# Kernel tuning notes

Measured on AMD Instinct MI355X. Metric: run time of the kernel, lower is better.

The kernel has to match this reference:

```python
import jax, jax.numpy as jnp
import numpy as np

H, I, BS = 4096, 14336, 128   # hidden, intermediate, quant blocksize
B, S = 4, 2048                # batch, seq_len


def _dequant(w_int, s, blocksize):
    # w_int: [in, out] int8-valued weights; s: [in//blocksize, out] per-block scales.
    # Each contiguous block of `blocksize` input rows shares one scale.
    return w_int.astype(jnp.float32) * jnp.repeat(s, blocksize, axis=0)


def setup_inputs() -> dict:
    key = jax.random.key(0)
    k = jax.random.split(key, 7)
    x = jax.random.normal(k[0], (B, S, H), dtype=jnp.float32)
    w0 = jax.random.randint(k[1], (H, I), -127, 128, dtype=jnp.int32)  # gate proj (int8 values)
    w1 = jax.random.randint(k[2], (H, I), -127, 128, dtype=jnp.int32)  # up proj
    w2 = jax.random.randint(k[3], (I, H), -127, 128, dtype=jnp.int32)  # down proj
    # small positive per-block scales, typical magnitude for int8 weight quant
    s0 = jax.random.uniform(k[4], (H // BS, I), dtype=jnp.float32) * 0.02 + 1e-3
    s1 = jax.random.uniform(k[5], (H // BS, I), dtype=jnp.float32) * 0.02 + 1e-3
    s2 = jax.random.uniform(k[6], (I // BS, H), dtype=jnp.float32) * 0.02 + 1e-3
    return {"x": x, "w0": w0, "w1": w1, "w2": w2,
            "s0": s0, "s1": s1, "s2": s2, "blocksize": BS}


def reference(x, w0, w1, w2, s0, s1, s2, blocksize):
    # Fused w8a16 gated MLP: out = (silu(x @ W0) * (x @ W1)) @ W2
    W0 = _dequant(w0, s0, blocksize)  # [H, I]
    W1 = _dequant(w1, s1, blocksize)  # [H, I]
    W2 = _dequant(w2, s2, blocksize)  # [I, H]
    g = jnp.einsum('bsh,hi->bsi', x, W0)   # gate
    u = jnp.einsum('bsh,hi->bsi', x, W1)   # up
    h = jax.nn.silu(g) * u                 # [B, S, I]
    return jnp.einsum('bsi,ih->bsh', h, W2)  # same shape as x
```

## Files before the change

kernel.cpp:

```cpp
#include <hip/hip_runtime.h>
#include <cstdint>

#define H_DIM 4096
#define I_DIM 14336
#define M_TOT 8192
#define NI_DIM (2 * I_DIM)

typedef __bf16 bf16_t;
typedef bf16_t bf16x8_t __attribute__((ext_vector_type(8)));
typedef float f32x4_t __attribute__((ext_vector_type(4)));

#define AS1 __attribute__((address_space(1)))
#define AS3 __attribute__((address_space(3)))

static __device__ __forceinline__ unsigned short f2bf(float f) {
  union { float f; unsigned int u; } v; v.f = f;
  unsigned int r = ((v.u >> 16) & 1u) + 0x7FFFu;
  return (unsigned short)((v.u + r) >> 16);
}

static __device__ __forceinline__ void gl2lds16(const void* g, void* l) {
  __builtin_amdgcn_global_load_lds((AS1 void*)(void*)g, (AS3 void*)l, 16, 0, 0);
}

__global__ void k_cvt_x(const float* __restrict__ x,
                        unsigned short* __restrict__ xb, long n4) {
  long i = (long)blockIdx.x * blockDim.x + threadIdx.x;
  const long stride = (long)gridDim.x * blockDim.x;
  for (; i < n4; i += stride) {
    float4 v = ((const float4*)x)[i];
    ushort4 o;
    o.x = f2bf(v.x); o.y = f2bf(v.y); o.z = f2bf(v.z); o.w = f2bf(v.w);
    ((ushort4*)xb)[i] = o;
  }
}

__global__ void k_dequant_t(const int* __restrict__ w, const float* __restrict__ s,
                            unsigned short* __restrict__ wt, int K, int N,
                            int ioff) {
  __shared__ __align__(16) float tile[64 * 68];
  const int n0 = blockIdx.x * 64;
  const int k0 = blockIdx.y * 64;
  const int t = threadIdx.x;
  const int tx = t & 15;
  const int ty = t >> 4;
#pragma unroll
  for (int i = 0; i < 4; ++i) {
    const long gk = k0 + i * 16 + ty;
    const int4 wv = *(const int4*)(w + gk * N + (n0 + tx * 4));
    const float4 sv = *(const float4*)(s + (gk >> 7) * (long)N + (n0 + tx * 4));
    float4 o;
    o.x = (float)wv.x * sv.x;
    o.y = (float)wv.y * sv.y;
    o.z = (float)wv.z * sv.z;
    o.w = (float)wv.w * sv.w;
    *(float4*)(&tile[(i * 16 + ty) * 68 + tx * 4]) = o;
  }
  __syncthreads();
  const int nl = t >> 2;
  const int kc = (t & 3) << 4;
  unsigned int pk[8];
#pragma unroll
  for (int j = 0; j < 8; ++j) {
    unsigned int lo = f2bf(tile[(kc + 2 * j) * 68 + nl]);
    unsigned int hi = f2bf(tile[(kc + 2 * j + 1) * 68 + nl]);
    pk[j] = lo | (hi << 16);
  }
  const int n = n0 + nl;
  const long orow = (ioff < 0) ? (long)n
                               : (long)(((n >> 4) << 5) + (n & 15) + ioff);
  const long base = orow * K + (k0 + kc);
  uint4* dst = (uint4*)(wt + base);
  dst[0] = make_uint4(pk[0], pk[1], pk[2], pk[3]);
  dst[1] = make_uint4(pk[4], pk[5], pk[6], pk[7]);
}

template <int KDIM, int EPI>
__global__ __launch_bounds__(512, 2) void k_gemm8(
    const unsigned short* __restrict__ A,
    const unsigned short* __restrict__ B,
    void* __restrict__ Cout, int Ntiles) {
  __shared__ __align__(16) unsigned short lds[65536];
  constexpr int KT = KDIM / 64;

  const int nwg = 32 * Ntiles;
  int id = blockIdx.x;
  id = (id & 7) * (nwg >> 3) + (id >> 3);
  const int per = 16 * Ntiles;
  const int grp = id / per;
  const int wi = id - grp * per;
  const int mt = grp * 16 + (wi & 15);
  const int nt = wi >> 4;
  const long m0 = (long)mt * 256;
  const long n0 = (long)nt * 256;

  const int t = threadIdx.x;
  const int lane = t & 63;
  const int wave = t >> 6;
  const int wm = wave >> 2;
  const int wn = wave & 3;

  const int srow = lane >> 3;
  const int scol = ((lane & 7) ^ srow) << 3;
  const unsigned short* pA = A + (m0 + wave * 16 + srow) * (long)KDIM + scol;
  const unsigned short* pB = B + (n0 + wave * 16 + srow) * (long)KDIM + scol;
  const int ldst = wave * 1024;

  const int lr = lane & 15;
  const int pch = ((lane >> 4) ^ (lane & 7)) << 3;
  int aof[4], bof[4];
#pragma unroll
  for (int mi = 0; mi < 4; ++mi)
    aof[mi] = wm * 8192 + (mi * 16 + lr) * 64 + pch;
#pragma unroll
  for (int nj = 0; nj < 4; ++nj)
    bof[nj] = 16384 + (wn >> 1) * 8192 +
              ((wn & 1) * 64 + nj * 16 + lr) * 64 + pch;

  auto stgA = [&](int tile, int half, int buf) {
    const long go = (long)half * 128 * KDIM + (long)tile * 64;
    unsigned short* d = &lds[buf * 32768 + half * 8192 + ldst];
    gl2lds16(pA + go, d);
    gl2lds16(pA + go + 8 * (long)KDIM, d + 512);
  };
  auto stgB = [&](int tile, int half, int buf) {
    const long go = (long)half * 128 * KDIM + (long)tile * 64;
    unsigned short* d = &lds[buf * 32768 + 16384 + half * 8192 + ldst];
    gl2lds16(pB + go, d);
    gl2lds16(pB + go + 8 * (long)KDIM, d + 512);
  };

  f32x4_t acc[8][4];
  const f32x4_t fz = {0.f, 0.f, 0.f, 0.f};
#pragma unroll
  for (int mi = 0; mi < 8; ++mi)
#pragma unroll
    for (int nj = 0; nj < 4; ++nj) acc[mi][nj] = fz;

  stgB(0, 0, 0); stgB(0, 1, 0);
  stgA(0, 0, 0); stgA(0, 1, 0);
  stgB(1, 0, 1); stgB(1, 1, 1);
  asm volatile("s_waitcnt vmcnt(4)" ::: "memory");
  __builtin_amdgcn_s_barrier();

  bf16x8_t af[4][2], b0[2][2], b1[2][2];

  for (int kt = 0; kt < KT; ++kt) {
    const int cb = kt & 1;
    const unsigned short* lb = &lds[cb * 32768];
    const bool pa = (kt + 1 < KT);
    const bool pb = (kt + 2 < KT);

#pragma unroll
    for (int mi = 0; mi < 4; ++mi) {
      af[mi][0] = *(const bf16x8_t*)(lb + aof[mi]);
      af[mi][1] = *(const bf16x8_t*)(lb + (aof[mi] ^ 32));
    }
#pragma unroll
    for (int nj = 0; nj < 2; ++nj) {
      b0[nj][0] = *(const bf16x8_t*)(lb + bof[nj]);
      b0[nj][1] = *(const bf16x8_t*)(lb + (bof[nj] ^ 32));
    }
    if (pa) stgA(kt + 1, 0, cb ^ 1);
    __builtin_amdgcn_s_barrier();
    asm volatile("s_waitcnt lgkmcnt(0)" ::: "memory");
    __builtin_amdgcn_sched_barrier(0);
    __builtin_amdgcn_s_setprio(1);
#pragma unroll
    for (int mi = 0; mi < 4; ++mi)
#pragma unroll
      for (int nj = 0; nj < 2; ++nj)
#pragma unroll
        for (int ks = 0; ks < 2; ++ks)
          acc[mi][nj] = __builtin_amdgcn_mfma_f32_16x16x32_bf16(
              af[mi][ks], b0[nj][ks], acc[mi][nj], 0, 0, 0);
    __builtin_amdgcn_s_setprio(0);
    __builtin_amdgcn_s_barrier();

#pragma unroll
    for (int nj = 0; nj < 2; ++nj) {
      b1[nj][0] = *(const bf16x8_t*)(lb + bof[2 + nj]);
      b1[nj][1] = *(const bf16x8_t*)(lb + (bof[2 + nj] ^ 32));
    }
    if (pa) stgA(kt + 1, 1, cb ^ 1);
    __builtin_amdgcn_s_barrier();
    asm volatile("s_waitcnt lgkmcnt(0)" ::: "memory");
    __builtin_amdgcn_sched_barrier(0);
    __builtin_amdgcn_s_setprio(1);
#pragma unroll
    for (int mi = 0; mi < 4; ++mi)
#pragma unroll
      for (int nj = 0; nj < 2; ++nj)
#pragma unroll
        for (int ks = 0; ks < 2; ++ks)
          acc[mi][2 + nj] = __builtin_amdgcn_mfma_f32_16x16x32_bf16(
              af[mi][ks], b1[nj][ks], acc[mi][2 + nj], 0, 0, 0);
    __builtin_amdgcn_s_setprio(0);
    __builtin_amdgcn_s_barrier();

#pragma unroll
    for (int mi = 0; mi < 4; ++mi) {
      af[mi][0] = *(const bf16x8_t*)(lb + (aof[mi] + 4096));
      af[mi][1] = *(const bf16x8_t*)(lb + ((aof[mi] + 4096) ^ 32));
    }
    if (pb) stgB(kt + 2, 0, cb);
    __builtin_amdgcn_s_barrier();
    asm volatile("s_waitcnt lgkmcnt(0)" ::: "memory");
    __builtin_amdgcn_sched_barrier(0);
    __builtin_amdgcn_s_setprio(1);
#pragma unroll
    for (int mi = 0; mi < 4; ++mi)
#pragma unroll
      for (int nj = 0; nj < 2; ++nj)
#pragma unroll
        for (int ks = 0; ks < 2; ++ks)
          acc[4 + mi][2 + nj] = __builtin_amdgcn_mfma_f32_16x16x32_bf16(
              af[mi][ks], b1[nj][ks], acc[4 + mi][2 + nj], 0, 0, 0);
    __builtin_amdgcn_s_setprio(0);
    __builtin_amdgcn_s_barrier();

    if (pb) stgB(kt + 2, 1, cb);
    __builtin_amdgcn_s_barrier();
    __builtin_amdgcn_s_setprio(1);
#pragma unroll
    for (int mi = 0; mi < 4; ++mi)
#pragma unroll
      for (int nj = 0; nj < 2; ++nj)
#pragma unroll
        for (int ks = 0; ks < 2; ++ks)
          acc[4 + mi][nj] = __builtin_amdgcn_mfma_f32_16x16x32_bf16(
              af[mi][ks], b0[nj][ks], acc[4 + mi][nj], 0, 0, 0);
    __builtin_amdgcn_s_setprio(0);
    if (pb)
      asm volatile("s_waitcnt vmcnt(4)" ::: "memory");
    else if (pa)
      asm volatile("s_waitcnt vmcnt(0)" ::: "memory");
    __builtin_amdgcn_s_barrier();
  }

  const long mr0 = m0 + wm * 128 + ((lane >> 4) << 2);
  if constexpr (EPI == 1) {
    unsigned short* h = (unsigned short*)Cout;
    const long col0 = (n0 >> 1) + wn * 32 + (lane & 15);
#pragma unroll
    for (int mi = 0; mi < 8; ++mi) {
#pragma unroll
      for (int k = 0; k < 2; ++k) {
        const long c = col0 + k * 16;
#pragma unroll
        for (int r = 0; r < 4; ++r) {
          const float gg = acc[mi][2 * k][r];
          const float uu = acc[mi][2 * k + 1][r];
          const float sg = gg / (1.0f + __expf(-gg));
          h[(mr0 + mi * 16 + r) * (long)I_DIM + c] = f2bf(sg * uu);
        }
      }
    }
  } else {
    float* o = (float*)Cout;
    const long col0 = n0 + wn * 64 + (lane & 15);
#pragma unroll
    for (int mi = 0; mi < 8; ++mi)
#pragma unroll
      for (int nj = 0; nj < 4; ++nj)
#pragma unroll
        for (int r = 0; r < 4; ++r)
          o[(mr0 + mi * 16 + r) * (long)H_DIM + (col0 + nj * 16)] =
              acc[mi][nj][r];
  }
}

extern "C" void kernel_launch(void* const* d_in, const int* in_sizes, int n_in,
                              void* d_out, int out_size, void* d_ws, size_t ws_size,
                              hipStream_t stream) {
  const float* x  = (const float*)d_in[0];
  const int* w0   = (const int*)d_in[1];
  const int* w1   = (const int*)d_in[2];
  const int* w2   = (const int*)d_in[3];
  const float* s0 = (const float*)d_in[4];
  const float* s1 = (const float*)d_in[5];
  const float* s2 = (const float*)d_in[6];
  float* out = (float*)d_out;

  char* p = (char*)d_ws;
  unsigned short* xb   = (unsigned short*)p;
  unsigned short* w01t = (unsigned short*)(p + (long)M_TOT * H_DIM * 2);
  unsigned short* hb   = (unsigned short*)(p + (long)M_TOT * H_DIM * 2 +
                                           (long)NI_DIM * H_DIM * 2);
  unsigned short* w2t  = (unsigned short*)p;

  k_cvt_x<<<8192, 256, 0, stream>>>(x, xb, (long)M_TOT * H_DIM / 4);

  k_dequant_t<<<dim3(I_DIM / 64, H_DIM / 64), 256, 0, stream>>>(
      w0, s0, w01t, H_DIM, I_DIM, 0);
  k_dequant_t<<<dim3(I_DIM / 64, H_DIM / 64), 256, 0, stream>>>(
      w1, s1, w01t, H_DIM, I_DIM, 16);

  k_gemm8<H_DIM, 1><<<(M_TOT / 256) * (NI_DIM / 256), 512, 0, stream>>>(
      xb, w01t, hb, NI_DIM / 256);

  k_dequant_t<<<dim3(H_DIM / 64, I_DIM / 64), 256, 0, stream>>>(
      w2, s2, w2t, I_DIM, H_DIM, -1);

  k_gemm8<I_DIM, 2><<<(M_TOT / 256) * (H_DIM / 256), 512, 0, stream>>>(
      hb, w2t, out, H_DIM / 256);
}
```

Baseline: 2.992 ms.

## Restructure GEMM k-loop into fewer barriers with separate A fragment registers

Reworks the inner k-loop schedule. Instead of four barrier-separated phases, it loads both B fragment sets and the first A half up front, issues both A prefetches together, and loads the second A half into a separate register set while MFMAs run. Most s_barrier and explicit lgkmcnt waits inside the iteration are removed, leaving one barrier before the B prefetch. The aim is to cut synchronisation overhead and overlap LDS reads with MFMA work, at the cost of more VGPRs and reliance on compiler-inserted waits for LDS/global ordering.

After: 2.967 ms. Within noise of the previous version (-0.8%).

```diff
diff --git a/kernel.cpp b/kernel.cpp
--- a/kernel.cpp
+++ b/kernel.cpp
@@ -143,49 +143,66 @@
   asm volatile("s_waitcnt vmcnt(4)" ::: "memory");
   __builtin_amdgcn_s_barrier();
 
-  bf16x8_t af[4][2], b0[2][2], b1[2][2];
-
   for (int kt = 0; kt < KT; ++kt) {
     const int cb = kt & 1;
     const unsigned short* lb = &lds[cb * 32768];
     const bool pa = (kt + 1 < KT);
     const bool pb = (kt + 2 < KT);
 
+    bf16x8_t af0[4][2], af1[4][2], b0[2][2], b1[2][2];
+
 #pragma unroll
     for (int mi = 0; mi < 4; ++mi) {
-      af[mi][0] = *(const bf16x8_t*)(lb + aof[mi]);
-      af[mi][1] = *(const bf16x8_t*)(lb + (aof[mi] ^ 32));
+      af0[mi][0] = *(const bf16x8_t*)(lb + aof[mi]);
+      af0[mi][1] = *(const bf16x8_t*)(lb + (aof[mi] ^ 32));
     }
 #pragma unroll
     for (int nj = 0; nj < 2; ++nj) {
       b0[nj][0] = *(const bf16x8_t*)(lb + bof[nj]);
       b0[nj][1] = *(const bf16x8_t*)(lb + (bof[nj] ^ 32));
     }
-    if (pa) stgA(kt + 1, 0, cb ^ 1);
-    __builtin_amdgcn_s_barrier();
-    asm volatile("s_waitcnt lgkmcnt(0)" ::: "memory");
-    __builtin_amdgcn_sched_barrier(0);
-    __builtin_amdgcn_s_setprio(1);
-#pragma unroll
-    for (int mi = 0; mi < 4; ++mi)
-#pragma unroll
-      for (int nj = 0; nj < 2; ++nj)
-#pragma unroll
-        for (int ks = 0; ks < 2; ++ks)
-          acc[mi][nj] = __builtin_amdgcn_mfma_f32_16x16x32_bf16(
-              af[mi][ks], b0[nj][ks], acc[mi][nj], 0, 0, 0);
-    __builtin_amdgcn_s_setprio(0);
-    __builtin_amdgcn_s_barrier();
-
 #pragma unroll
     for (int nj = 0; nj < 2; ++nj) {
       b1[nj][0] = *(const bf16x8_t*)(lb + bof[2 + nj]);
       b1[nj][1] = *(const bf16x8_t*)(lb + (bof[2 + nj] ^ 32));
     }
-    if (pa) stgA(kt + 1, 1, cb ^ 1);
+    if (pa) { stgA(kt + 1, 0, cb ^ 1); stgA(kt + 1, 1, cb ^ 1); }
+    __builtin_amdgcn_sched_barrier(0);
+
+    __builtin_amdgcn_s_setprio(1);
+#pragma unroll
+    for (int mi = 0; mi < 4; ++mi)
+#pragma unroll
+      for (int nj = 0; nj < 2; ++nj)
+#pragma unroll
+        for (int ks = 0; ks < 2; ++ks)
+          acc[mi][nj] = __builtin_amdgcn_mfma_f32_16x16x32_bf16(
+              af0[mi][ks], b0[nj][ks], acc[mi][nj], 0, 0, 0);
+    __builtin_amdgcn_s_setprio(0);
+    __builtin_amdgcn_sched_barrier(0);
+
+#pragma unroll
+    for (int mi = 0; mi < 4; ++mi) {
+      af1[mi][0] = *(const bf16x8_t*)(lb + (aof[mi] + 4096));
+      af1[mi][1] = *(const bf16x8_t*)(lb + ((aof[mi] + 4096) ^ 32));
+    }
+    __builtin_amdgcn_sched_barrier(0);
+
+    __builtin_amdgcn_s_setprio(1);
+#pragma unroll
+    for (int mi = 0; mi < 4; ++mi)
+#pragma unroll
+      for (int nj = 0; nj < 2; ++nj)
+#pragma unroll
+        for (int ks = 0; ks < 2; ++ks)
+          acc[mi][2 + nj] = __builtin_amdgcn_mfma_f32_16x16x32_bf16(
+              af0[mi][ks], b1[nj][ks], acc[mi][2 + nj], 0, 0, 0);
+    __builtin_amdgcn_s_setprio(0);
+
     __builtin_amdgcn_s_barrier();
-    asm volatile("s_waitcnt lgkmcnt(0)" ::: "memory");
-    __builtin_amdgcn_sched_barrier(0);
+    if (pb) { stgB(kt + 2, 0, cb); stgB(kt + 2, 1, cb); }
+    __builtin_amdgcn_sched_barrier(0);
+
     __builtin_amdgcn_s_setprio(1);
 #pragma unroll
     for (int mi = 0; mi < 4; ++mi)
@@ -193,44 +210,18 @@
       for (int nj = 0; nj < 2; ++nj)
 #pragma unroll
         for (int ks = 0; ks < 2; ++ks)
-          acc[mi][2 + nj] = __builtin_amdgcn_mfma_f32_16x16x32_bf16(
-              af[mi][ks], b1[nj][ks], acc[mi][2 + nj], 0, 0, 0);
+          acc[4 + mi][2 + nj] = __builtin_amdgcn_mfma_f32_16x16x32_bf16(
+              af1[mi][ks], b1[nj][ks], acc[4 + mi][2 + nj], 0, 0, 0);
+#pragma unroll
+    for (int mi = 0; mi < 4; ++mi)
+#pragma unroll
+      for (int nj = 0; nj < 2; ++nj)
+#pragma unroll
+        for (int ks = 0; ks < 2; ++ks)
+          acc[4 + mi][nj] = __builtin_amdgcn_mfma_f32_16x16x32_bf16(
+              af1[mi][ks], b0[nj][ks], acc[4 + mi][nj], 0, 0, 0);
     __builtin_amdgcn_s_setprio(0);
-    __builtin_amdgcn_s_barrier();
-
-#pragma unroll
-    for (int mi = 0; mi < 4; ++mi) {
-      af[mi][0] = *(const bf16x8_t*)(lb + (aof[mi] + 4096));
-      af[mi][1] = *(const bf16x8_t*)(lb + ((aof[mi] + 4096) ^ 32));
-    }
-    if (pb) stgB(kt + 2, 0, cb);
-    __builtin_amdgcn_s_barrier();
-    asm volatile("s_waitcnt lgkmcnt(0)" ::: "memory");
-    __builtin_amdgcn_sched_barrier(0);
-    __builtin_amdgcn_s_setprio(1);
-#pragma unroll
-    for (int mi = 0; mi < 4; ++mi)
-#pragma unroll
-      for (int nj = 0; nj < 2; ++nj)
-#pragma unroll
-        for (int ks = 0; ks < 2; ++ks)
-          acc[4 + mi][2 + nj] = __builtin_amdgcn_mfma_f32_16x16x32_bf16(
-              af[mi][ks], b1[nj][ks], acc[4 + mi][2 + nj], 0, 0, 0);
-    __builtin_amdgcn_s_setprio(0);
-    __builtin_amdgcn_s_barrier();
-
-    if (pb) stgB(kt + 2, 1, cb);
-    __builtin_amdgcn_s_barrier();
-    __builtin_amdgcn_s_setprio(1);
-#pragma unroll
-    for (int mi = 0; mi < 4; ++mi)
-#pragma unroll
-      for (int nj = 0; nj < 2; ++nj)
-#pragma unroll
-        for (int ks = 0; ks < 2; ++ks)
-          acc[4 + mi][nj] = __builtin_amdgcn_mfma_f32_16x16x32_bf16(
-              af[mi][ks], b0[nj][ks], acc[4 + mi][nj], 0, 0, 0);
-    __builtin_amdgcn_s_setprio(0);
+
     if (pb)
       asm volatile("s_waitcnt vmcnt(4)" ::: "memory");
     else if (pa)
```
